# Kernel optimization log

Hardware: AMD Instinct MI355X
Metric: run time of the kernel (lower is better)

Reference implementation:

```python
import jax, jax.numpy as jnp
import numpy as np

S, B, H = 2048, 64, 512


def setup_inputs() -> dict:
    key = jax.random.key(0)
    k1, k2, k3 = jax.random.split(key, 3)
    hidden = jax.random.normal(k1, (1, B, H), dtype=jnp.float32)          # decoder hidden [1,B,H]
    encoder_outputs = jax.random.normal(k2, (S, B, 2 * H), dtype=jnp.float32)  # [S,B,2H]
    W = jax.random.normal(k3, (H, 2 * H), dtype=jnp.float32) * 0.02       # Linear(2H -> H) weight
    b = jnp.zeros((H,), dtype=jnp.float32)
    return {"hidden": hidden, "encoder_outputs": encoder_outputs, "W": W, "b": b}


def reference(hidden, encoder_outputs, W, b):
    # 'general' method: project encoder outputs 2H -> H, then score against decoder hidden.
    proj = jnp.einsum('sbf,hf->bsh', encoder_outputs, W) + b   # [B,S,H]
    scores = jnp.einsum('bh,bsh->bs', hidden[0], proj)[:, None, :]  # [B,1,S]
    # legacy softmax(transpose(0,2)).transpose(0,2) == softmax over seq axis
    return jax.nn.softmax(scores, axis=-1)
```

## Files before the change

### kernel.cpp

```cpp
#include <hip/hip_runtime.h>


#define SS 2048
#define BB 64
#define HH 512
#define FF 1024

__device__ __forceinline__ void fma4(float4& a, float s, const float4& w) {
    a.x += s * w.x; a.y += s * w.y; a.z += s * w.z; a.w += s * w.w;
}

__global__ __launch_bounds__(256) void proj_vec(const float* __restrict__ hidden,
                                                const float* __restrict__ W,
                                                float* __restrict__ v) {
    __shared__ float h0[HH];
    __shared__ float h1[HH];
    const int t  = threadIdx.x;
    const int b0 = blockIdx.x * 2;
    const int b1 = b0 + 1;
    for (int i = t; i < HH; i += 256) {
        h0[i] = hidden[b0 * HH + i];
        h1[i] = hidden[b1 * HH + i];
    }
    __syncthreads();

    const float4* W4 = (const float4*)W;
    float4 acc0 = {0.f, 0.f, 0.f, 0.f};
    float4 acc1 = {0.f, 0.f, 0.f, 0.f};

    #pragma unroll 4
    for (int h = 0; h < HH; h += 4) {
        float4 ha = *(const float4*)&h0[h];
        float4 hb = *(const float4*)&h1[h];
        float4 w0 = W4[(h + 0) * 256 + t];
        float4 w1 = W4[(h + 1) * 256 + t];
        float4 w2 = W4[(h + 2) * 256 + t];
        float4 w3 = W4[(h + 3) * 256 + t];
        fma4(acc0, ha.x, w0); fma4(acc0, ha.y, w1); fma4(acc0, ha.z, w2); fma4(acc0, ha.w, w3);
        fma4(acc1, hb.x, w0); fma4(acc1, hb.y, w1); fma4(acc1, hb.z, w2); fma4(acc1, hb.w, w3);
    }
    float4* v4 = (float4*)v;
    v4[b0 * 256 + t] = acc0;
    v4[b1 * 256 + t] = acc1;
}

#define KS 8
__global__ __launch_bounds__(256) void score_k(const float* __restrict__ enc,
                                               const float* __restrict__ v,
                                               float* __restrict__ scores) {
    const int wave = blockIdx.x * 4 + (threadIdx.x >> 6);
    const int lane = threadIdx.x & 63;
    const int b    = wave & (BB - 1);
    const int s0   = (wave >> 6) * KS;

    const float4* v4 = (const float4*)(v + (size_t)b * FF);
    const float4 v0 = v4[lane +   0];
    const float4 v1 = v4[lane +  64];
    const float4 v2 = v4[lane + 128];
    const float4 v3 = v4[lane + 192];

    #pragma unroll
    for (int k = 0; k < KS; ++k) {
        const int s = s0 + k;
        const float4* e4 = (const float4*)(enc + ((size_t)s * BB + b) * FF);
        float4 e0 = e4[lane +   0];
        float4 e1 = e4[lane +  64];
        float4 e2 = e4[lane + 128];
        float4 e3 = e4[lane + 192];
        float acc = e0.x * v0.x + e0.y * v0.y + e0.z * v0.z + e0.w * v0.w
                  + e1.x * v1.x + e1.y * v1.y + e1.z * v1.z + e1.w * v1.w
                  + e2.x * v2.x + e2.y * v2.y + e2.z * v2.z + e2.w * v2.w
                  + e3.x * v3.x + e3.y * v3.y + e3.z * v3.z + e3.w * v3.w;
        #pragma unroll
        for (int off = 32; off; off >>= 1) acc += __shfl_down(acc, off, 64);
        if (lane == 0) scores[(size_t)b * SS + s] = acc;
    }
}

__global__ __launch_bounds__(256) void softmax_k(const float* __restrict__ scores,
                                                 float* __restrict__ out) {
    __shared__ float sm[4];
    const int b = blockIdx.x, t = threadIdx.x;
    const int w = t >> 6, lane = t & 63;

    const float4* r4 = (const float4*)(scores + (size_t)b * SS);
    float4 a = r4[t];
    float4 c = r4[t + 256];

    float m = fmaxf(fmaxf(fmaxf(a.x, a.y), fmaxf(a.z, a.w)),
                    fmaxf(fmaxf(c.x, c.y), fmaxf(c.z, c.w)));
    #pragma unroll
    for (int off = 32; off; off >>= 1) m = fmaxf(m, __shfl_down(m, off, 64));
    if (lane == 0) sm[w] = m;
    __syncthreads();
    m = fmaxf(fmaxf(sm[0], sm[1]), fmaxf(sm[2], sm[3]));
    __syncthreads();

    a.x = __expf(a.x - m); a.y = __expf(a.y - m); a.z = __expf(a.z - m); a.w = __expf(a.w - m);
    c.x = __expf(c.x - m); c.y = __expf(c.y - m); c.z = __expf(c.z - m); c.w = __expf(c.w - m);

    float ssum = a.x + a.y + a.z + a.w + c.x + c.y + c.z + c.w;
    #pragma unroll
    for (int off = 32; off; off >>= 1) ssum += __shfl_down(ssum, off, 64);
    if (lane == 0) sm[w] = ssum;
    __syncthreads();
    const float inv = 1.0f / (sm[0] + sm[1] + sm[2] + sm[3]);

    a.x *= inv; a.y *= inv; a.z *= inv; a.w *= inv;
    c.x *= inv; c.y *= inv; c.z *= inv; c.w *= inv;

    float4* o4 = (float4*)(out + (size_t)b * SS);
    o4[t]       = a;
    o4[t + 256] = c;
}

extern "C" void kernel_launch(void* const* d_in, const int* in_sizes, int n_in,
                              void* d_out, int out_size, void* d_ws, size_t ws_size,
                              hipStream_t stream) {
    const float* hidden = (const float*)d_in[0];
    const float* enc    = (const float*)d_in[1];
    const float* W      = (const float*)d_in[2];
    float* out    = (float*)d_out;
    float* v      = (float*)d_ws;
    float* scores = v + BB * FF;

    proj_vec<<<BB / 2, 256, 0, stream>>>(hidden, W, v);
    score_k<<<(SS * BB) / (4 * KS), 256, 0, stream>>>(enc, v, scores);
    softmax_k<<<BB, 256, 0, stream>>>(scores, out);
}
```

Before: 732.9 us.

## Split projection over hidden chunks, use nontemporal loads, and raise score rows per wave

The hidden-to-feature projection is split into 4 hidden chunks across 256 blocks instead of 32 blocks. Partial vectors go to workspace, and the score kernel sums them when it starts. The score kernel now uses nontemporal loads for the streamed encoder outputs and processes 16 sequence rows per wave with partial unrolling. The aim is more parallelism in the small projection kernel and less cache pollution from the large encoder read. The cost is extra workspace traffic for the partial vectors.

```diff
diff --git a/kernel.cpp b/kernel.cpp
--- a/kernel.cpp
+++ b/kernel.cpp
@@ -6,67 +6,56 @@
 #define HH 512
 #define FF 1024
 
-__device__ __forceinline__ void fma4(float4& a, float s, const float4& w) {
-    a.x += s * w.x; a.y += s * w.y; a.z += s * w.z; a.w += s * w.w;
+typedef float vf4 __attribute__((ext_vector_type(4)));
+
+__global__ __launch_bounds__(256) void proj_partial(const float* __restrict__ hidden,
+                                                    const float* __restrict__ W,
+                                                    float* __restrict__ vp) {
+    __shared__ float hs[128];
+    const int t  = threadIdx.x;
+    const int b  = blockIdx.x >> 2;
+    const int hc = blockIdx.x & 3;
+    const int h0 = hc * 128;
+    if (t < 128) hs[t] = hidden[b * HH + h0 + t];
+    __syncthreads();
+
+    const vf4* W4 = (const vf4*)W;
+    vf4 acc = {0.f, 0.f, 0.f, 0.f};
+    #pragma unroll 4
+    for (int i = 0; i < 128; ++i) {
+        acc += hs[i] * W4[(h0 + i) * 256 + t];
+    }
+    ((vf4*)vp)[(hc * BB + b) * 256 + t] = acc;
 }
 
-__global__ __launch_bounds__(256) void proj_vec(const float* __restrict__ hidden,
-                                                const float* __restrict__ W,
-                                                float* __restrict__ v) {
-    __shared__ float h0[HH];
-    __shared__ float h1[HH];
-    const int t  = threadIdx.x;
-    const int b0 = blockIdx.x * 2;
-    const int b1 = b0 + 1;
-    for (int i = t; i < HH; i += 256) {
-        h0[i] = hidden[b0 * HH + i];
-        h1[i] = hidden[b1 * HH + i];
-    }
-    __syncthreads();
-
-    const float4* W4 = (const float4*)W;
-    float4 acc0 = {0.f, 0.f, 0.f, 0.f};
-    float4 acc1 = {0.f, 0.f, 0.f, 0.f};
-
-    #pragma unroll 4
-    for (int h = 0; h < HH; h += 4) {
-        float4 ha = *(const float4*)&h0[h];
-        float4 hb = *(const float4*)&h1[h];
-        float4 w0 = W4[(h + 0) * 256 + t];
-        float4 w1 = W4[(h + 1) * 256 + t];
-        float4 w2 = W4[(h + 2) * 256 + t];
-        float4 w3 = W4[(h + 3) * 256 + t];
-        fma4(acc0, ha.x, w0); fma4(acc0, ha.y, w1); fma4(acc0, ha.z, w2); fma4(acc0, ha.w, w3);
-        fma4(acc1, hb.x, w0); fma4(acc1, hb.y, w1); fma4(acc1, hb.z, w2); fma4(acc1, hb.w, w3);
-    }
-    float4* v4 = (float4*)v;
-    v4[b0 * 256 + t] = acc0;
-    v4[b1 * 256 + t] = acc1;
-}
-
-#define KS 8
+#define KS 16
 __global__ __launch_bounds__(256) void score_k(const float* __restrict__ enc,
-                                               const float* __restrict__ v,
+                                               const float* __restrict__ vp,
                                                float* __restrict__ scores) {
     const int wave = blockIdx.x * 4 + (threadIdx.x >> 6);
     const int lane = threadIdx.x & 63;
     const int b    = wave & (BB - 1);
     const int s0   = (wave >> 6) * KS;
 
-    const float4* v4 = (const float4*)(v + (size_t)b * FF);
-    const float4 v0 = v4[lane +   0];
-    const float4 v1 = v4[lane +  64];
-    const float4 v2 = v4[lane + 128];
-    const float4 v3 = v4[lane + 192];
+    const vf4* vp4 = (const vf4*)vp;
+    vf4 v0 = {0,0,0,0}, v1 = {0,0,0,0}, v2 = {0,0,0,0}, v3 = {0,0,0,0};
+    #pragma unroll
+    for (int hc = 0; hc < 4; ++hc) {
+        const vf4* p = vp4 + (size_t)(hc * BB + b) * 256;
+        v0 += p[lane +   0];
+        v1 += p[lane +  64];
+        v2 += p[lane + 128];
+        v3 += p[lane + 192];
+    }
 
-    #pragma unroll
+    #pragma unroll 4
     for (int k = 0; k < KS; ++k) {
         const int s = s0 + k;
-        const float4* e4 = (const float4*)(enc + ((size_t)s * BB + b) * FF);
-        float4 e0 = e4[lane +   0];
-        float4 e1 = e4[lane +  64];
-        float4 e2 = e4[lane + 128];
-        float4 e3 = e4[lane + 192];
+        const vf4* e4 = (const vf4*)(enc + ((size_t)s * BB + b) * FF);
+        vf4 e0 = __builtin_nontemporal_load(e4 + lane +   0);
+        vf4 e1 = __builtin_nontemporal_load(e4 + lane +  64);
+        vf4 e2 = __builtin_nontemporal_load(e4 + lane + 128);
+        vf4 e3 = __builtin_nontemporal_load(e4 + lane + 192);
         float acc = e0.x * v0.x + e0.y * v0.y + e0.z * v0.z + e0.w * v0.w
                   + e1.x * v1.x + e1.y * v1.y + e1.z * v1.z + e1.w * v1.w
                   + e2.x * v2.x + e2.y * v2.y + e2.z * v2.z + e2.w * v2.w
@@ -83,9 +72,9 @@
     const int b = blockIdx.x, t = threadIdx.x;
     const int w = t >> 6, lane = t & 63;
 
-    const float4* r4 = (const float4*)(scores + (size_t)b * SS);
-    float4 a = r4[t];
-    float4 c = r4[t + 256];
+    const vf4* r4 = (const vf4*)(scores + (size_t)b * SS);
+    vf4 a = r4[t];
+    vf4 c = r4[t + 256];
 
     float m = fmaxf(fmaxf(fmaxf(a.x, a.y), fmaxf(a.z, a.w)),
                     fmaxf(fmaxf(c.x, c.y), fmaxf(c.z, c.w)));
@@ -106,10 +95,10 @@
     __syncthreads();
     const float inv = 1.0f / (sm[0] + sm[1] + sm[2] + sm[3]);
 
-    a.x *= inv; a.y *= inv; a.z *= inv; a.w *= inv;
-    c.x *= inv; c.y *= inv; c.z *= inv; c.w *= inv;
+    a *= inv;
+    c *= inv;
 
-    float4* o4 = (float4*)(out + (size_t)b * SS);
+    vf4* o4 = (vf4*)(out + (size_t)b * SS);
     o4[t]       = a;
     o4[t + 256] = c;
 }
@@ -121,10 +110,10 @@
     const float* enc    = (const float*)d_in[1];
     const float* W      = (const float*)d_in[2];
     float* out    = (float*)d_out;
-    float* v      = (float*)d_ws;
-    float* scores = v + BB * FF;
+    float* vp     = (float*)d_ws;
+    float* scores = vp + 4 * BB * FF;
 
-    proj_vec<<<BB / 2, 256, 0, stream>>>(hidden, W, v);
-    score_k<<<(SS * BB) / (4 * KS), 256, 0, stream>>>(enc, v, scores);
+    proj_partial<<<BB * 4, 256, 0, stream>>>(hidden, W, vp);
+    score_k<<<(SS / KS) * BB / 4, 256, 0, stream>>>(enc, vp, scores);
     softmax_k<<<BB, 256, 0, stream>>>(scores, out);
 }
```

After: 672.7 us. -8.2%, faster.
